# Performance work log

Measured on AMD Instinct MI355X. Metric: run time of the kernel, lower is better.

Reference implementation:

```python
import jax, jax.numpy as jnp
import numpy as np

BATCH, SEQ_LEN, VEC_DIM, WIDTH = 64, 256, 512, 3


def setup_inputs() -> dict:
    key = jax.random.key(0)
    k = jax.random.split(key, 8)
    F0r = jax.random.normal(k[0], (BATCH, SEQ_LEN, VEC_DIM), jnp.float32)
    F1r = jax.random.normal(k[1], (BATCH, SEQ_LEN, VEC_DIM), jnp.float32)
    sent0_mask = (jax.random.uniform(k[2], (BATCH, SEQ_LEN)) < 0.9).astype(jnp.float32)
    sent1_mask = (jax.random.uniform(k[3], (BATCH, SEQ_LEN)) < 0.9).astype(jnp.float32)
    # nn.Parameter(torch.randn(seq_len, vec_dim))
    W0 = jax.random.normal(k[4], (SEQ_LEN, VEC_DIM), jnp.float32)
    W1 = jax.random.normal(k[5], (SEQ_LEN, VEC_DIM), jnp.float32)
    # Conv2d(2, 1, kernel_size=(WIDTH, 1)) default init: U(-1/sqrt(fan_in), +)
    bound = 1.0 / np.sqrt(2 * WIDTH * 1)
    conv_w = jax.random.uniform(k[6], (1, 2, WIDTH, 1), jnp.float32, -bound, bound)
    conv_b = jax.random.uniform(k[7], (1,), jnp.float32, -bound, bound)
    return dict(F0r=F0r, F1r=F1r, sent0_mask=sent0_mask, sent1_mask=sent1_mask,
                W0=W0, W1=W1, conv_w=conv_w, conv_b=conv_b)


def _conv_tanh_pool(x, conv_w, conv_b):
    # x: [B, 2, S, D]; conv pad (WIDTH-1, 0) -> [B, 1, S+WIDTH-1, D]
    y = jax.lax.conv_general_dilated(
        x, conv_w, window_strides=(1, 1),
        padding=((WIDTH - 1, WIDTH - 1), (0, 0)),
        dimension_numbers=('NCHW', 'OIHW', 'NCHW'))
    y = jnp.tanh(y + conv_b[None, :, None, None])
    # AvgPool2d kernel (WIDTH,1), stride 1 -> [B, 1, S, D]
    y = jax.lax.reduce_window(y, 0.0, jax.lax.add,
                              (1, 1, WIDTH, 1), (1, 1, 1, 1), 'VALID') / WIDTH
    return y[:, 0]  # squeeze channel -> [B, S, D]


def reference(F0r, F1r, sent0_mask, sent1_mask, W0, W1, conv_w, conv_b):
    # masking is in-place in the torch code, so masked F0/F1 feed the conv too
    F0 = F0r * sent0_mask[:, :, None]  # [B, S, D]
    F1 = F1r * sent1_mask[:, :, None]
    # pairwise L2 via ||u-v||^2 = ||u||^2 + ||v||^2 - 2 u.v (avoids [B,S,S,D])
    sq0 = jnp.sum(F0 * F0, axis=-1)  # [B, S]
    sq1 = jnp.sum(F1 * F1, axis=-1)
    cross = jnp.einsum('bid,bjd->bij', F0, F1)  # [B, S, S]
    d2 = jnp.maximum(sq0[:, :, None] + sq1[:, None, :] - 2.0 * cross, 0.0)
    norm = jnp.where(d2 > 0, jnp.sqrt(jnp.where(d2 > 0, d2, 1.0)), 0.0)
    A = 1.0 / (1.0 + norm)  # [B, S, S]
    F0a = jnp.einsum('bij,id->bjd', A, W0)  # A^T @ W0
    F1a = jnp.einsum('bij,jd->bid', A, W1)  # A @ W1
    x0 = jnp.stack([F0, F0a], axis=1)  # [B, 2, S, D]
    x1 = jnp.stack([F1, F1a], axis=1)
    out0 = _conv_tanh_pool(x0, conv_w, conv_b)
    out1 = _conv_tanh_pool(x1, conv_w, conv_b)
    return out0, out1
```

## Files before the change

kernel.cpp:

```cpp
#include <hip/hip_runtime.h>

typedef unsigned short u16;
typedef __attribute__((ext_vector_type(8))) short short8;
typedef __attribute__((ext_vector_type(4))) float f32x4;

__device__ inline u16 f2bf(float f) {
    union { float f; unsigned u; } v; v.f = f;
    unsigned u = v.u;
    unsigned r = (u + 0x7FFFu + ((u >> 16) & 1u)) >> 16;
    return (u16)r;
}
__device__ inline float bf2f(u16 h) {
    union { unsigned u; float f; } v; v.u = ((unsigned)h) << 16;
    return v.f;
}
__device__ inline float ftanh(float x) {
    float e = __expf(2.f * x);
    return 1.f - 2.f / (e + 1.f);
}
__device__ inline float4 bf4f(ushort4 u) {
    float4 f; f.x = bf2f(u.x); f.y = bf2f(u.y); f.z = bf2f(u.z); f.w = bf2f(u.w);
    return f;
}

typedef const __attribute__((address_space(1))) void* gas_ptr;
typedef __attribute__((address_space(3))) void* las_ptr;
__device__ __forceinline__ void gl2lds16(const u16* g, u16* l) {
    __builtin_amdgcn_global_load_lds((gas_ptr)(const void*)g, (las_ptr)(void*)l, 16, 0, 0);
}

__global__ __launch_bounds__(128) void prep_kernel(
    const float* __restrict__ F0r, const float* __restrict__ F1r,
    const float* __restrict__ m0, const float* __restrict__ m1,
    const float* __restrict__ W0, const float* __restrict__ W1,
    u16* __restrict__ F0b, u16* __restrict__ F1b,
    u16* __restrict__ WT0, u16* __restrict__ WT1,
    float* __restrict__ sq0, float* __restrict__ sq1)
{
    int bx = blockIdx.x;
    int t = threadIdx.x;
    if (bx >= 16384) {
        int idx = (bx - 16384) * 128 + t;
        int a = idx >> 17;
        int r = idx & 131071;
        int s = r >> 9, d = r & 511;
        const float* W = a ? W1 : W0;
        u16* WT = a ? WT1 : WT0;
        WT[d * 256 + s] = f2bf(W[r]);
        return;
    }
    int bs = bx;
    size_t base = (size_t)bs * 512 + t * 4;
    float mk0 = m0[bs], mk1 = m1[bs];
    float4 v0 = *(const float4*)(F0r + base);
    float4 v1 = *(const float4*)(F1r + base);
    v0.x *= mk0; v0.y *= mk0; v0.z *= mk0; v0.w *= mk0;
    v1.x *= mk1; v1.y *= mk1; v1.z *= mk1; v1.w *= mk1;
    ushort4 u0; u0.x = f2bf(v0.x); u0.y = f2bf(v0.y); u0.z = f2bf(v0.z); u0.w = f2bf(v0.w);
    ushort4 u1; u1.x = f2bf(v1.x); u1.y = f2bf(v1.y); u1.z = f2bf(v1.z); u1.w = f2bf(v1.w);
    *(ushort4*)(F0b + base) = u0;
    *(ushort4*)(F1b + base) = u1;
    float s0p = v0.x*v0.x + v0.y*v0.y + v0.z*v0.z + v0.w*v0.w;
    float s1p = v1.x*v1.x + v1.y*v1.y + v1.z*v1.z + v1.w*v1.w;
    #pragma unroll
    for (int off = 32; off > 0; off >>= 1) {
        s0p += __shfl_xor(s0p, off);
        s1p += __shfl_xor(s1p, off);
    }
    __shared__ float red0[2], red1[2];
    if ((t & 63) == 0) { red0[t >> 6] = s0p; red1[t >> 6] = s1p; }
    __syncthreads();
    if (t == 0) { sq0[bs] = red0[0] + red0[1]; sq1[bs] = red1[0] + red1[1]; }
}

__global__ __launch_bounds__(256) void gemm_cross_kernel(
    const u16* __restrict__ F0b, const u16* __restrict__ F1b,
    const float* __restrict__ sq0, const float* __restrict__ sq1,
    u16* __restrict__ Abf, u16* __restrict__ ATbf)
{
    __shared__ __align__(16) u16 smem[4 * 8192];

    int b = blockIdx.y;
    int i0 = (blockIdx.x >> 2) * 64, j0 = (blockIdx.x & 3) * 64;
    const u16* Ap = F0b + (size_t)b * 131072;
    const u16* Bp = F1b + (size_t)b * 131072;
    const float* sqR = sq0 + b * 256;
    const float* sqC = sq1 + b * 256;

    const int t = threadIdx.x;
    const int lane = t & 63, w = t >> 6;
    const int wm = w >> 1, wn = w & 1;
    const int q = lane >> 4, lm = lane & 15;

#define STAGE_AB(bufo, k0) do {                                                \
    _Pragma("unroll")                                                          \
    for (int i_ = 0; i_ < 4; ++i_) {                                           \
        int idx_ = i_ * 256 + t;                                               \
        int row_ = idx_ >> 4, seg_ = idx_ & 15;                                \
        int ss_  = seg_ ^ (row_ & 7);                                          \
        int lo_  = (bufo) + (i_ * 256 + w * 64) * 8;         \
        gl2lds16(Ap + (size_t)(i0 + row_) * 512 + (k0) + ss_ * 8,              \
                 &smem[lo_]);                                                  \
        gl2lds16(Bp + (size_t)(j0 + row_) * 512 + (k0) + ss_ * 8,              \
                 &smem[lo_ + 8192]);                                           \
    } } while (0)

    f32x4 acc[2][2];
    #pragma unroll
    for (int x = 0; x < 2; ++x)
        #pragma unroll
        for (int y = 0; y < 2; ++y)
            acc[x][y] = (f32x4){0.f, 0.f, 0.f, 0.f};

    STAGE_AB(0, 0);

    #pragma unroll
    for (int c = 0; c < 4; ++c) {
        __syncthreads();
        if (c < 3)
            STAGE_AB(((c + 1) & 1) * 16384, (c + 1) * 128);
        const int cb = (c & 1) * 16384;
        #pragma unroll
        for (int ks = 0; ks < 128; ks += 32) {
            short8 af[2], bfr[2];
            #pragma unroll
            for (int x = 0; x < 2; ++x) {
                int ra = wm * 32 + x * 16 + lm;
                int rb = wn * 32 + x * 16 + lm;
                int su = (((ks >> 3) + q) ^ (lm & 7)) * 8;
                af[x]  = *(const short8*)&smem[cb + ra * 128 + su];
                bfr[x] = *(const short8*)&smem[cb + 8192 + rb * 128 + su];
            }
            #pragma unroll
            for (int x = 0; x < 2; ++x)
                #pragma unroll
                for (int y = 0; y < 2; ++y)
                    acc[x][y] = __builtin_amdgcn_mfma_f32_16x16x32_bf16(
                        af[x], bfr[y], acc[x][y], 0, 0, 0);
        }
    }
    __syncthreads();
#undef STAGE_AB

    u16 (*Ct)[136] = (u16(*)[136])smem;
    #pragma unroll
    for (int x = 0; x < 2; ++x) {
        #pragma unroll
        for (int r = 0; r < 4; ++r) {
            int ir = wm * 32 + x * 16 + q * 4 + r;
            float si = sqR[i0 + ir];
            #pragma unroll
            for (int y = 0; y < 2; ++y) {
                int jc = wn * 32 + y * 16 + lm;
                float d2 = si + sqC[j0 + jc] - 2.f * acc[x][y][r];
                d2 = fmaxf(d2, 0.f);
                float a = 1.f / (1.f + sqrtf(d2));
                Ct[ir][jc] = f2bf(a);
            }
        }
    }
    __syncthreads();

    u16* Aout  = Abf  + (size_t)b * 65536;
    u16* ATout = ATbf + (size_t)b * 65536;
    int ii = t >> 2;
    int c0 = (t & 3) * 16;
    #pragma unroll
    for (int c = 0; c < 4; ++c) {
        ushort4 v = *(ushort4*)&Ct[ii][c0 + c * 4];
        *(ushort4*)&Aout[(size_t)(i0 + ii) * 256 + j0 + c0 + c * 4] = v;
    }
    #pragma unroll
    for (int c = 0; c < 4; ++c) {
        ushort4 v;
        v.x = Ct[c0 + c * 4 + 0][ii];
        v.y = Ct[c0 + c * 4 + 1][ii];
        v.z = Ct[c0 + c * 4 + 2][ii];
        v.w = Ct[c0 + c * 4 + 3][ii];
        *(ushort4*)&ATout[(size_t)(j0 + ii) * 256 + i0 + c0 + c * 4] = v;
    }
}

__global__ __launch_bounds__(256) void fa_conv_kernel(
    const u16* __restrict__ Abf, const u16* __restrict__ ATbf,
    const u16* __restrict__ WT0, const u16* __restrict__ WT1,
    const u16* __restrict__ F0b, const u16* __restrict__ F1b,
    const float* __restrict__ cw, const float* __restrict__ cb,
    float* __restrict__ out)
{
    __shared__ __align__(16) u16 Al[36][264];
    __shared__ __align__(16) u16 BlBuf[2 * 8192];
    __shared__ __align__(16) u16 Fl[36][132];

    int b = blockIdx.y, side = blockIdx.z;
    int s0 = blockIdx.x * 32;
    const u16* Ap = (side ? Abf : ATbf) + (size_t)b * 65536;
    const u16* WT = side ? WT1 : WT0;
    const u16* Fb = (side ? F1b : F0b) + (size_t)b * 131072;
    float* o = out + (size_t)side * 8388608 + (size_t)b * 131072;

    const int t = threadIdx.x;
    const int lane = t & 63, w = t >> 6;
    const int q = lane >> 4, lm = lane & 15;

#define STAGE_B(bufo, nn, kb) do {                                             \
    _Pragma("unroll")                                                          \
    for (int i_ = 0; i_ < 4; ++i_) {                                           \
        int idx_ = i_ * 256 + t;                                               \
        int r_ = idx_ >> 3, seg_ = idx_ & 7;                                   \
        int ss_ = seg_ ^ (r_ & 7);                                             \
        gl2lds16(WT + (size_t)((nn) + r_) * 256 + (kb) + ss_ * 8,              \
                 &BlBuf[(bufo) + (i_ * 256 + w * 64) * 8]);                    \
    } } while (0)

    #pragma unroll
    for (int i = 0; i < 5; ++i) {
        int idx = i * 256 + t;
        if (idx < 1152) {
            int r = idx >> 5;
            int seg = idx & 31;
            int s = s0 - 2 + r;
            uint4 v = {0u, 0u, 0u, 0u};
            if ((unsigned)s < 256u)
                v = *(const uint4*)(Ap + (size_t)s * 256 + seg * 8);
            *(uint4*)&Al[r][seg * 8] = v;
        }
    }

    const u16* aRow[3];
    aRow[0] = &Al[lm][0];
    aRow[1] = &Al[16 + lm][0];
    aRow[2] = &Al[(lm < 4) ? (32 + lm) : 0][0];

    float w00 = cw[0], w01 = cw[1], w02 = cw[2];
    float w10 = cw[3], w11 = cw[4], w12 = cw[5];
    float bias = cb[0];
    const float third = 1.f / 3.f;
    const int g = t >> 5;
    const int dl = (t & 31) * 4;

    STAGE_B(0, 0, 0);

    for (int n0 = 0; n0 < 512; n0 += 128) {
        f32x4 acc[3][2];
        #pragma unroll
        for (int x = 0; x < 3; ++x)
            #pragma unroll
            for (int y = 0; y < 2; ++y)
                acc[x][y] = (f32x4){0.f, 0.f, 0.f, 0.f};

        #pragma unroll
        for (int kb_i = 0; kb_i < 4; ++kb_i) {
            __syncthreads();
            if (kb_i < 3)
                STAGE_B(((kb_i + 1) & 1) * 8192, n0, (kb_i + 1) * 64);
            const int cbuf = (kb_i & 1) * 8192;
            const int kb = kb_i * 64;
            #pragma unroll
            for (int ks = 0; ks < 64; ks += 32) {
                short8 af[3], bfr[2];
                #pragma unroll
                for (int x = 0; x < 3; ++x)
                    af[x] = *(const short8*)(aRow[x] + kb + ks + q * 8);
                #pragma unroll
                for (int y = 0; y < 2; ++y) {
                    int rb = w * 32 + y * 16 + lm;
                    int su = (((ks >> 3) + q) ^ (lm & 7)) * 8;
                    bfr[y] = *(const short8*)&BlBuf[cbuf + rb * 64 + su];
                }
                #pragma unroll
                for (int x = 0; x < 3; ++x)
                    #pragma unroll
                    for (int y = 0; y < 2; ++y)
                        acc[x][y] = __builtin_amdgcn_mfma_f32_16x16x32_bf16(
                            af[x], bfr[y], acc[x][y], 0, 0, 0);
            }
        }

        #pragma unroll
        for (int x = 0; x < 3; ++x)
            #pragma unroll
            for (int r = 0; r < 4; ++r) {
                int m = x * 16 + q * 4 + r;
                if (m < 36) {
                    #pragma unroll
                    for (int y = 0; y < 2; ++y)
                        Fl[m][w * 32 + y * 16 + lm] = f2bf(acc[x][y][r]);
                }
            }
        __syncthreads();

        if (n0 < 384)
            STAGE_B(0, n0 + 128, 0);

        float4 f[8], a[8];
        #pragma unroll
        for (int k = 0; k < 8; ++k) {
            int s = s0 + g * 4 - 2 + k;
            if ((unsigned)s < 256u)
                f[k] = bf4f(*(const ushort4*)(Fb + (size_t)s * 512 + n0 + dl));
            else
                f[k] = make_float4(0.f, 0.f, 0.f, 0.f);
            a[k] = bf4f(*(const ushort4*)&Fl[g * 4 + k][dl]);
        }
        float4 ty[6];
        #pragma unroll
        for (int k = 0; k < 6; ++k) {
            float4 y;
            y.x = bias + w00*f[k].x + w01*f[k+1].x + w02*f[k+2].x + w10*a[k].x + w11*a[k+1].x + w12*a[k+2].x;
            y.y = bias + w00*f[k].y + w01*f[k+1].y + w02*f[k+2].y + w10*a[k].y + w11*a[k+1].y + w12*a[k+2].y;
            y.z = bias + w00*f[k].z + w01*f[k+1].z + w02*f[k+2].z + w10*a[k].z + w11*a[k+1].z + w12*a[k+2].z;
            y.w = bias + w00*f[k].w + w01*f[k+1].w + w02*f[k+2].w + w10*a[k].w + w11*a[k+1].w + w12*a[k+2].w;
            y.x = ftanh(y.x); y.y = ftanh(y.y); y.z = ftanh(y.z); y.w = ftanh(y.w);
            ty[k] = y;
        }
        #pragma unroll
        for (int r = 0; r < 4; ++r) {
            float4 res;
            res.x = (ty[r].x + ty[r+1].x + ty[r+2].x) * third;
            res.y = (ty[r].y + ty[r+1].y + ty[r+2].y) * third;
            res.z = (ty[r].z + ty[r+1].z + ty[r+2].z) * third;
            res.w = (ty[r].w + ty[r+1].w + ty[r+2].w) * third;
            *(float4*)(o + (size_t)(s0 + g * 4 + r) * 512 + n0 + dl) = res;
        }
    }
#undef STAGE_B
}

extern "C" void kernel_launch(void* const* d_in, const int* in_sizes, int n_in,
                              void* d_out, int out_size, void* d_ws, size_t ws_size,
                              hipStream_t stream)
{
    const float* F0r = (const float*)d_in[0];
    const float* F1r = (const float*)d_in[1];
    const float* m0  = (const float*)d_in[2];
    const float* m1  = (const float*)d_in[3];
    const float* W0  = (const float*)d_in[4];
    const float* W1  = (const float*)d_in[5];
    const float* cw  = (const float*)d_in[6];
    const float* cb  = (const float*)d_in[7];
    float* out = (float*)d_out;

    char* ws = (char*)d_ws;
    u16* F0b   = (u16*)(ws);
    u16* F1b   = (u16*)(ws + 16777216);
    u16* Abf   = (u16*)(ws + 33554432);
    u16* ATbf  = (u16*)(ws + 41943040);
    float* sq0 = (float*)(ws + 50331648);
    float* sq1 = (float*)(ws + 50397184);
    u16* WT0   = (u16*)(ws + 50462720);
    u16* WT1   = (u16*)(ws + 50724864);

    prep_kernel<<<18432, 128, 0, stream>>>(F0r, F1r, m0, m1, W0, W1,
                                           F0b, F1b, WT0, WT1, sq0, sq1);
    gemm_cross_kernel<<<dim3(16, 64), 256, 0, stream>>>(F0b, F1b, sq0, sq1, Abf, ATbf);
    fa_conv_kernel<<<dim3(8, 64, 2), 256, 0, stream>>>(Abf, ATbf, WT0, WT1,
                                                       F0b, F1b, cw, cb, out);
}
```

Baseline: 201.4 us.

## Tile W transpose through LDS, use fast rcp/sqrt, prefetch conv F loads

The W-to-bf16 transpose in prep_kernel now stages 32x64 tiles in shared memory, so both the global reads and the global writes are coalesced. This replaces 2048 scattered-write blocks with 128 tiled ones. The distance-to-affinity and tanh math switch to the hardware rcp/sqrt intrinsics, which are less accurate than IEEE division and sqrt. The conv epilogue now issues its global F row loads before the accumulator store to LDS and the barrier, so that load latency overlaps with that work.

```diff
diff --git a/kernel.cpp b/kernel.cpp
--- a/kernel.cpp
+++ b/kernel.cpp
@@ -14,9 +14,11 @@
     union { unsigned u; float f; } v; v.u = ((unsigned)h) << 16;
     return v.f;
 }
+__device__ inline float frcp(float x) { return __builtin_amdgcn_rcpf(x); }
+__device__ inline float fsqrt(float x) { return __builtin_amdgcn_sqrtf(x); }
 __device__ inline float ftanh(float x) {
     float e = __expf(2.f * x);
-    return 1.f - 2.f / (e + 1.f);
+    return 1.f - 2.f * frcp(e + 1.f);
 }
 __device__ inline float4 bf4f(ushort4 u) {
     float4 f; f.x = bf2f(u.x); f.y = bf2f(u.y); f.z = bf2f(u.z); f.w = bf2f(u.w);
@@ -40,13 +42,33 @@
     int bx = blockIdx.x;
     int t = threadIdx.x;
     if (bx >= 16384) {
-        int idx = (bx - 16384) * 128 + t;
-        int a = idx >> 17;
-        int r = idx & 131071;
-        int s = r >> 9, d = r & 511;
+        __shared__ u16 Wl[64][40];
+        int idx2 = bx - 16384;
+        int a = idx2 >> 6;
+        int tile = idx2 & 63;
+        int s0 = (tile >> 3) * 32, d0 = (tile & 7) * 64;
         const float* W = a ? W1 : W0;
         u16* WT = a ? WT1 : WT0;
-        WT[d * 256 + s] = f2bf(W[r]);
+        #pragma unroll
+        for (int i = 0; i < 4; ++i) {
+            int idx = i * 512 + t * 4;
+            int sl = idx >> 6, dl = idx & 63;
+            float4 v = *(const float4*)(W + (size_t)(s0 + sl) * 512 + d0 + dl);
+            Wl[dl + 0][sl] = f2bf(v.x);
+            Wl[dl + 1][sl] = f2bf(v.y);
+            Wl[dl + 2][sl] = f2bf(v.z);
+            Wl[dl + 3][sl] = f2bf(v.w);
+        }
+        __syncthreads();
+        #pragma unroll
+        for (int i = 0; i < 4; ++i) {
+            int idx = i * 512 + t * 4;
+            int dl = idx >> 5, sl = idx & 31;
+            ushort4 v;
+            v.x = Wl[dl][sl + 0]; v.y = Wl[dl][sl + 1];
+            v.z = Wl[dl][sl + 2]; v.w = Wl[dl][sl + 3];
+            *(ushort4*)(WT + (size_t)(d0 + dl) * 256 + s0 + sl) = v;
+        }
         return;
     }
     int bs = bx;
@@ -154,7 +176,7 @@
                 int jc = wn * 32 + y * 16 + lm;
                 float d2 = si + sqC[j0 + jc] - 2.f * acc[x][y][r];
                 d2 = fmaxf(d2, 0.f);
-                float a = 1.f / (1.f + sqrtf(d2));
+                float a = frcp(1.f + fsqrt(d2));
                 Ct[ir][jc] = f2bf(a);
             }
         }
@@ -277,6 +299,15 @@
             }
         }
 
+        ushort4 frg[8];
+        #pragma unroll
+        for (int k = 0; k < 8; ++k) {
+            int s = s0 + g * 4 - 2 + k;
+            ushort4 z = {0, 0, 0, 0};
+            frg[k] = ((unsigned)s < 256u)
+                   ? *(const ushort4*)(Fb + (size_t)s * 512 + n0 + dl) : z;
+        }
+
         #pragma unroll
         for (int x = 0; x < 3; ++x)
             #pragma unroll
@@ -296,11 +327,7 @@
         float4 f[8], a[8];
         #pragma unroll
         for (int k = 0; k < 8; ++k) {
-            int s = s0 + g * 4 - 2 + k;
-            if ((unsigned)s < 256u)
-                f[k] = bf4f(*(const ushort4*)(Fb + (size_t)s * 512 + n0 + dl));
-            else
-                f[k] = make_float4(0.f, 0.f, 0.f, 0.f);
+            f[k] = bf4f(frg[k]);
             a[k] = bf4f(*(const ushort4*)&Fl[g * 4 + k][dl]);
         }
         float4 ty[6];
@@ -351,7 +378,7 @@
     u16* WT0   = (u16*)(ws + 50462720);
     u16* WT1   = (u16*)(ws + 50724864);
 
-    prep_kernel<<<18432, 128, 0, stream>>>(F0r, F1r, m0, m1, W0, W1,
+    prep_kernel<<<16512, 128, 0, stream>>>(F0r, F1r, m0, m1, W0, W1,
                                            F0b, F1b, WT0, WT1, sq0, sq1);
     gemm_cross_kernel<<<dim3(16, 64), 256, 0, stream>>>(F0b, F1b, sq0, sq1, Abf, ATbf);
     fa_conv_kernel<<<dim3(8, 64, 2), 256, 0, stream>>>(Abf, ATbf, WT0, WT1,
```

After: 184.3 us. 1.09x faster.
